# Kernel optimization log

Measured on AMD Instinct MI355X. Metric: run time of the kernel, lower is better.

Reference implementation:

```python
import jax, jax.numpy as jnp
import numpy as np

N = 50000      # nodes
E = 800000     # edges (avg degree 16)
G = 128        # graphs in batch
IN = 128       # in_channels
H = 128        # hidden_dim
C = 10         # num_classes


def setup_inputs() -> dict:
    key = jax.random.key(0)
    ks = jax.random.split(key, 8)
    x = jax.random.normal(ks[0], (N, IN), dtype=jnp.float32)
    edge_index = jax.random.randint(ks[1], (2, E), 0, N)
    edge_attr = jax.random.uniform(ks[2], (E,), dtype=jnp.float32)
    batch = jnp.sort(jax.random.randint(ks[3], (N,), 0, G))
    def glorot(k, fan_in, fan_out):
        return jax.random.normal(k, (fan_in, fan_out), dtype=jnp.float32) / np.float32(np.sqrt(fan_in))
    return {
        "x": x,
        "edge_index": edge_index,
        "edge_attr": edge_attr,
        "batch": batch,
        "W1": glorot(ks[4], IN, H), "b1": jnp.zeros((H,), jnp.float32),
        "W2": glorot(ks[5], H, H), "b2": jnp.zeros((H,), jnp.float32),
        "W3": glorot(ks[6], H, C), "b3": jnp.zeros((C,), jnp.float32),
    }


def gcn_conv(x, src, dst, ew, W, b, n):
    # symmetric GCN normalization (self-loops already appended, weight 1)
    deg = jax.ops.segment_sum(ew, dst, num_segments=n)            # [N]
    dinv = jnp.where(deg > 0, jax.lax.rsqrt(deg), 0.0)
    norm = dinv[src] * ew * dinv[dst]                             # [E+N]
    h = x @ W                                                     # [N, out]
    agg = jax.ops.segment_sum(h[src] * norm[:, None], dst, num_segments=n)
    return agg + b


def reference(x, edge_index, edge_attr, batch, W1, b1, W2, b2, W3, b3):
    n = x.shape[0]
    loop = jnp.arange(n)
    src = jnp.concatenate([edge_index[0], loop])
    dst = jnp.concatenate([edge_index[1], loop])
    ew = jnp.concatenate([edge_attr, jnp.ones((n,), edge_attr.dtype)])
    h = jax.nn.relu(gcn_conv(x, src, dst, ew, W1, b1, n))   # dropout is identity in eval
    h = jax.nn.relu(gcn_conv(h, src, dst, ew, W2, b2, n))
    h = gcn_conv(h, src, dst, ew, W3, b3, n)                 # [N, C]
    # global mean pool over graphs
    sums = jax.ops.segment_sum(h, batch, num_segments=G)     # [G, C]
    cnt = jax.ops.segment_sum(jnp.ones((n,), h.dtype), batch, num_segments=G)
    pooled = sums / jnp.maximum(cnt, 1.0)[:, None]
    return jax.nn.log_softmax(pooled, axis=1)
```

## Files before the change

kernel.cpp:

```cpp
#include <hip/hip_runtime.h>

#define NN 50000
#define NE 800000
#define NG 128
#define DIM 128
#define CO 10
#define CAP 64
#define NB 2048

typedef unsigned long long ull;
typedef unsigned short ushort;
typedef unsigned int uint;

static __device__ __forceinline__ ushort f2bf(float f) {
    uint u = __float_as_uint(f);
    uint r = (u + 0x7FFF + ((u >> 16) & 1)) >> 16;
    return (ushort)r;
}
#define EWS (1.0f / 65535.0f)

__global__ void k_ell(const int* __restrict__ src, const int* __restrict__ dst,
                      const float* __restrict__ ew, int* __restrict__ cnt,
                      uint* __restrict__ ell) {
    int e = blockIdx.x * blockDim.x + threadIdx.x;
    if (e >= NE) return;
    int d = dst[e], s = src[e];
    int slot = atomicAdd(&cnt[d], 1);
    if (slot < CAP) {
        uint w16 = (uint)__float2uint_rn(ew[e] * 65535.0f);
        ell[(size_t)d * CAP + slot] = (w16 << 16) | (uint)s;
    }
}

__global__ __launch_bounds__(256) void k_deg(const int* __restrict__ cnt,
                                             const uint* __restrict__ ell,
                                             float* __restrict__ dinv) {
    int node = blockIdx.x * 4 + (threadIdx.x >> 6);
    int lane = threadIdx.x & 63;
    if (node >= NN) return;
    int n = cnt[node];
    float w = 0.0f;
    if (lane < n) w = (float)(ell[(size_t)node * CAP + lane] >> 16) * EWS;
#pragma unroll
    for (int off = 32; off; off >>= 1) w += __shfl_down(w, off);
    if (lane == 0) dinv[node] = rsqrtf(1.0f + w);
}

__global__ __launch_bounds__(256) void k_gemm128(const void* __restrict__ Ain, int abf,
                                                 const float* __restrict__ W,
                                                 const float* __restrict__ dinv,
                                                 ushort* __restrict__ C, int M) {
    __shared__ float As[64][33];
    __shared__ float Bs[32][132];
    int tid = threadIdx.x;
    int block_row = blockIdx.x * 64;
    int tx = tid & 15;
    int ty = tid >> 4;
    int r0 = ty * 4;
    int c1 = tx * 4, c2 = 64 + tx * 4;
    float acc[4][8];
#pragma unroll
    for (int i = 0; i < 4; i++)
#pragma unroll
        for (int j = 0; j < 8; j++) acc[i][j] = 0.0f;

    for (int k0 = 0; k0 < 128; k0 += 32) {
        if (abf) {
            const ushort* Ab = (const ushort*)Ain;
            int ar = tid >> 2;
            int ac = (tid & 3) * 8;
            int grow = block_row + ar;
            if (grow >= M) grow = M - 1;
            uint4 v = *(const uint4*)&Ab[(size_t)grow * 128 + k0 + ac];
            As[ar][ac + 0] = __uint_as_float(v.x << 16);
            As[ar][ac + 1] = __uint_as_float(v.x & 0xffff0000u);
            As[ar][ac + 2] = __uint_as_float(v.y << 16);
            As[ar][ac + 3] = __uint_as_float(v.y & 0xffff0000u);
            As[ar][ac + 4] = __uint_as_float(v.z << 16);
            As[ar][ac + 5] = __uint_as_float(v.z & 0xffff0000u);
            As[ar][ac + 6] = __uint_as_float(v.w << 16);
            As[ar][ac + 7] = __uint_as_float(v.w & 0xffff0000u);
        } else {
            const float* Af = (const float*)Ain;
#pragma unroll
            for (int l = 0; l < 2; l++) {
                int idx = tid + l * 256;
                int ar = idx >> 3;
                int ac = (idx & 7) * 4;
                int grow = block_row + ar;
                if (grow >= M) grow = M - 1;
                float4 v = *(const float4*)&Af[(size_t)grow * 128 + k0 + ac];
                As[ar][ac + 0] = v.x; As[ar][ac + 1] = v.y;
                As[ar][ac + 2] = v.z; As[ar][ac + 3] = v.w;
            }
        }
#pragma unroll
        for (int l = 0; l < 4; l++) {
            int idx = tid + l * 256;
            int br = idx >> 5;
            int bc = (idx & 31) * 4;
            float4 v = *(const float4*)&W[(size_t)(k0 + br) * 128 + bc];
            *(float4*)&Bs[br][bc] = v;
        }
        __syncthreads();
#pragma unroll
        for (int kk = 0; kk < 32; kk++) {
            float a0 = As[r0 + 0][kk];
            float a1 = As[r0 + 1][kk];
            float a2 = As[r0 + 2][kk];
            float a3 = As[r0 + 3][kk];
            float4 bl = *(float4*)&Bs[kk][c1];
            float4 bh = *(float4*)&Bs[kk][c2];
            acc[0][0] += a0 * bl.x; acc[0][1] += a0 * bl.y; acc[0][2] += a0 * bl.z; acc[0][3] += a0 * bl.w;
            acc[0][4] += a0 * bh.x; acc[0][5] += a0 * bh.y; acc[0][6] += a0 * bh.z; acc[0][7] += a0 * bh.w;
            acc[1][0] += a1 * bl.x; acc[1][1] += a1 * bl.y; acc[1][2] += a1 * bl.z; acc[1][3] += a1 * bl.w;
            acc[1][4] += a1 * bh.x; acc[1][5] += a1 * bh.y; acc[1][6] += a1 * bh.z; acc[1][7] += a1 * bh.w;
            acc[2][0] += a2 * bl.x; acc[2][1] += a2 * bl.y; acc[2][2] += a2 * bl.z; acc[2][3] += a2 * bl.w;
            acc[2][4] += a2 * bh.x; acc[2][5] += a2 * bh.y; acc[2][6] += a2 * bh.z; acc[2][7] += a2 * bh.w;
            acc[3][0] += a3 * bl.x; acc[3][1] += a3 * bl.y; acc[3][2] += a3 * bl.z; acc[3][3] += a3 * bl.w;
            acc[3][4] += a3 * bh.x; acc[3][5] += a3 * bh.y; acc[3][6] += a3 * bh.z; acc[3][7] += a3 * bh.w;
        }
        __syncthreads();
    }
#pragma unroll
    for (int i = 0; i < 4; i++) {
        int grow = block_row + r0 + i;
        if (grow < M) {
            float di = dinv[grow];
            ushort4 u1, u2;
            u1.x = f2bf(di * acc[i][0]); u1.y = f2bf(di * acc[i][1]);
            u1.z = f2bf(di * acc[i][2]); u1.w = f2bf(di * acc[i][3]);
            u2.x = f2bf(di * acc[i][4]); u2.y = f2bf(di * acc[i][5]);
            u2.z = f2bf(di * acc[i][6]); u2.w = f2bf(di * acc[i][7]);
            *(ushort4*)&C[(size_t)grow * 128 + c1] = u1;
            *(ushort4*)&C[(size_t)grow * 128 + c2] = u2;
        }
    }
}

__global__ __launch_bounds__(256) void k_gemm10(const ushort* __restrict__ A,
                                                const float* __restrict__ W3,
                                                const float* __restrict__ dinv,
                                                float* __restrict__ C3, int M) {
    __shared__ float Ws[1280];
    int tid = threadIdx.x;
    for (int i = tid; i < 1280; i += 256) Ws[i] = W3[i];
    __syncthreads();
    int col = tid & 15;
    int rloc = tid >> 4;
    int row = blockIdx.x * 16 + rloc;
    if (row >= M || col >= 10) return;
    const ushort* a = &A[(size_t)row * 128];
    float acc = 0.0f;
#pragma unroll
    for (int k = 0; k < 128; k += 4) {
        ushort4 av = *(const ushort4*)&a[k];
        acc += __uint_as_float((uint)av.x << 16) * Ws[(k + 0) * 10 + col];
        acc += __uint_as_float((uint)av.y << 16) * Ws[(k + 1) * 10 + col];
        acc += __uint_as_float((uint)av.z << 16) * Ws[(k + 2) * 10 + col];
        acc += __uint_as_float((uint)av.w << 16) * Ws[(k + 3) * 10 + col];
    }
    C3[(size_t)row * 10 + col] = dinv[row] * acc;
}

__global__ __launch_bounds__(256) void k_gather128(const int* __restrict__ cnt,
                                                   const uint* __restrict__ ell,
                                                   const float* __restrict__ dinv,
                                                   const ushort* __restrict__ h,
                                                   const float* __restrict__ b,
                                                   ushort* __restrict__ outp) {
    int node = blockIdx.x * 4 + (threadIdx.x >> 6);
    int lane = threadIdx.x & 63;
    if (node >= NN) return;
    int n = cnt[node];
    uint hp = *(const uint*)&h[(size_t)node * 128 + lane * 2];
    float ax = __uint_as_float(hp << 16);
    float ay = __uint_as_float(hp & 0xffff0000u);
    uint rec = ell[(size_t)node * CAP + lane];
    int ce = (int)(rec & 0xffffu);
    float we = (float)(rec >> 16) * EWS;
    int j = 0;
    for (; j + 3 < n; j += 4) {
        int s0 = __shfl(ce, j + 0), s1 = __shfl(ce, j + 1);
        int s2 = __shfl(ce, j + 2), s3 = __shfl(ce, j + 3);
        float w0 = __shfl(we, j + 0), w1 = __shfl(we, j + 1);
        float w2 = __shfl(we, j + 2), w3 = __shfl(we, j + 3);
        uint p0 = *(const uint*)&h[(size_t)s0 * 128 + lane * 2];
        uint p1 = *(const uint*)&h[(size_t)s1 * 128 + lane * 2];
        uint p2 = *(const uint*)&h[(size_t)s2 * 128 + lane * 2];
        uint p3 = *(const uint*)&h[(size_t)s3 * 128 + lane * 2];
        ax += w0 * __uint_as_float(p0 << 16) + w1 * __uint_as_float(p1 << 16)
            + w2 * __uint_as_float(p2 << 16) + w3 * __uint_as_float(p3 << 16);
        ay += w0 * __uint_as_float(p0 & 0xffff0000u) + w1 * __uint_as_float(p1 & 0xffff0000u)
            + w2 * __uint_as_float(p2 & 0xffff0000u) + w3 * __uint_as_float(p3 & 0xffff0000u);
    }
    for (; j < n; j++) {
        int s0 = __shfl(ce, j);
        float w0 = __shfl(we, j);
        uint p0 = *(const uint*)&h[(size_t)s0 * 128 + lane * 2];
        ax += w0 * __uint_as_float(p0 << 16);
        ay += w0 * __uint_as_float(p0 & 0xffff0000u);
    }
    float di = dinv[node];
    ax = fmaxf(di * ax + b[lane * 2 + 0], 0.0f);
    ay = fmaxf(di * ay + b[lane * 2 + 1], 0.0f);
    uint o = ((uint)f2bf(ay) << 16) | (uint)f2bf(ax);
    *(uint*)&outp[(size_t)node * 128 + lane * 2] = o;
}

__global__ __launch_bounds__(256) void k_pool_node(const int* __restrict__ cnt,
                                                   const uint* __restrict__ ell,
                                                   const float* __restrict__ dinv,
                                                   const float* __restrict__ z,
                                                   const int* __restrict__ batch,
                                                   float* __restrict__ partial) {
    __shared__ float ls[NG * CO + NG];
    for (int i = threadIdx.x; i < NG * CO + NG; i += 256) ls[i] = 0.0f;
    __syncthreads();
    int lane = threadIdx.x & 63;
    int gwave = blockIdx.x * 4 + (threadIdx.x >> 6);
    for (int node = gwave; node < NN; node += NB * 4) {
        int n = cnt[node];
        float w = 0.0f; int s = 0;
        if (lane < n) {
            uint rec = ell[(size_t)node * CAP + lane];
            s = (int)(rec & 0xffffu);
            w = (float)(rec >> 16) * EWS;
        } else if (lane == n) {
            s = node;
            w = 1.0f;
        }
        const float* zp = &z[(size_t)s * 10];
        float v[10];
#pragma unroll
        for (int f = 0; f < 10; f++) v[f] = w * zp[f];
#pragma unroll
        for (int off = 32; off; off >>= 1) {
#pragma unroll
            for (int f = 0; f < 10; f++) v[f] += __shfl_down(v[f], off);
        }
        if (lane == 0) {
            int g = batch[node];
            float di = dinv[node];
            float* lp = &ls[g * 10];
#pragma unroll
            for (int f = 0; f < 10; f++) atomicAdd(&lp[f], di * v[f]);
            atomicAdd(&ls[NG * CO + g], 1.0f);
        }
    }
    __syncthreads();
    float* pb = &partial[(size_t)blockIdx.x * (NG * CO + NG)];
    for (int i = threadIdx.x; i < NG * CO + NG; i += 256) pb[i] = ls[i];
}

__global__ __launch_bounds__(256) void k_pool_final(const float* __restrict__ partial,
                                                    const float* __restrict__ b3,
                                                    float* __restrict__ out) {
    __shared__ float red[4][11];
    int g = blockIdx.x;
    int t = threadIdx.x;
    int lane = t & 63, wv = t >> 6;
    float v[10]; float c = 0.0f;
#pragma unroll
    for (int f = 0; f < 10; f++) v[f] = 0.0f;
    for (int b = t; b < NB; b += 256) {
        const float* pb = &partial[(size_t)b * (NG * CO + NG)];
#pragma unroll
        for (int f = 0; f < 10; f++) v[f] += pb[g * 10 + f];
        c += pb[NG * CO + g];
    }
#pragma unroll
    for (int off = 32; off; off >>= 1) {
#pragma unroll
        for (int f = 0; f < 10; f++) v[f] += __shfl_down(v[f], off);
        c += __shfl_down(c, off);
    }
    if (lane == 0) {
#pragma unroll
        for (int f = 0; f < 10; f++) red[wv][f] = v[f];
        red[wv][10] = c;
    }
    __syncthreads();
    if (t == 0) {
        float p[10], m = -1e30f;
        float cc = red[0][10] + red[1][10] + red[2][10] + red[3][10];
        cc = fmaxf(cc, 1.0f);
#pragma unroll
        for (int f = 0; f < 10; f++) {
            p[f] = (red[0][f] + red[1][f] + red[2][f] + red[3][f]) / cc + b3[f];
            m = fmaxf(m, p[f]);
        }
        float ssum = 0.0f;
#pragma unroll
        for (int f = 0; f < 10; f++) ssum += __expf(p[f] - m);
        float lse = m + __logf(ssum);
#pragma unroll
        for (int f = 0; f < 10; f++) out[g * 10 + f] = p[f] - lse;
    }
}

extern "C" void kernel_launch(void* const* d_in, const int* in_sizes, int n_in,
                              void* d_out, int out_size, void* d_ws, size_t ws_size,
                              hipStream_t stream) {
    const float* x     = (const float*)d_in[0];
    const int*   ei    = (const int*)d_in[1];
    const float* ea    = (const float*)d_in[2];
    const int*   batch = (const int*)d_in[3];
    const float* W1    = (const float*)d_in[4];
    const float* b1    = (const float*)d_in[5];
    const float* W2    = (const float*)d_in[6];
    const float* b2    = (const float*)d_in[7];
    const float* W3    = (const float*)d_in[8];
    const float* b3    = (const float*)d_in[9];
    float* out = (float*)d_out;
    float* ws  = (float*)d_ws;

    const int* esrc = ei;
    const int* edst = ei + NE;

    ushort* hb      = (ushort*)ws;
    ushort* gb      = (ushort*)(ws + 3200000);
    float*  z       = ws + 6400000;
    float*  dinv    = ws + 6900000;
    int*    cnt     = (int*)(ws + 6950000);
    uint*   ell     = (uint*)(ws + 7000000);
    float*  partial = (float*)hb;

    hipMemsetAsync(cnt, 0, NN * sizeof(int), stream);
    k_ell<<<(NE + 255) / 256, 256, 0, stream>>>(esrc, edst, ea, cnt, ell);
    k_deg<<<(NN + 3) / 4, 256, 0, stream>>>(cnt, ell, dinv);

    k_gemm128<<<(NN + 63) / 64, 256, 0, stream>>>(x, 0, W1, dinv, hb, NN);
    k_gather128<<<(NN + 3) / 4, 256, 0, stream>>>(cnt, ell, dinv, hb, b1, gb);

    k_gemm128<<<(NN + 63) / 64, 256, 0, stream>>>(gb, 1, W2, dinv, hb, NN);
    k_gather128<<<(NN + 3) / 4, 256, 0, stream>>>(cnt, ell, dinv, hb, b2, gb);

    k_gemm10<<<(NN + 15) / 16, 256, 0, stream>>>(gb, W3, dinv, z, NN);
    k_pool_node<<<NB, 256, 0, stream>>>(cnt, ell, dinv, z, batch, partial);
    k_pool_final<<<NG, 256, 0, stream>>>(partial, b3, out);
}
```

Measured before the change: 325.7 us.

## Replace FP32 SIMT GEMM with bf16 MFMA GEMM using pre-transposed weights

Swaps the shared-memory tiled FP32 GEMM for a matrix-core kernel that uses the 16x16x32 bf16 MFMA instruction, with operands loaded straight from global memory. Two small kernels convert W1 and W2 into transposed bf16 copies in workspace so each lane can load contiguous 8-element B fragments. The first layer's fp32 input is rounded to bf16 in registers, which lowers precision. Output stores become scalar 16-bit writes per lane instead of vectorized ones.

```diff
diff --git a/kernel.cpp b/kernel.cpp
--- a/kernel.cpp
+++ b/kernel.cpp
@@ -11,6 +11,8 @@
 typedef unsigned long long ull;
 typedef unsigned short ushort;
 typedef unsigned int uint;
+typedef __attribute__((ext_vector_type(8))) short short8;
+typedef __attribute__((ext_vector_type(4))) float floatx4;
 
 static __device__ __forceinline__ ushort f2bf(float f) {
     uint u = __float_as_uint(f);
@@ -46,94 +48,58 @@
     if (lane == 0) dinv[node] = rsqrtf(1.0f + w);
 }
 
-__global__ __launch_bounds__(256) void k_gemm128(const void* __restrict__ Ain, int abf,
-                                                 const float* __restrict__ W,
-                                                 const float* __restrict__ dinv,
-                                                 ushort* __restrict__ C, int M) {
-    __shared__ float As[64][33];
-    __shared__ float Bs[32][132];
-    int tid = threadIdx.x;
-    int block_row = blockIdx.x * 64;
-    int tx = tid & 15;
-    int ty = tid >> 4;
-    int r0 = ty * 4;
-    int c1 = tx * 4, c2 = 64 + tx * 4;
-    float acc[4][8];
-#pragma unroll
-    for (int i = 0; i < 4; i++)
-#pragma unroll
-        for (int j = 0; j < 8; j++) acc[i][j] = 0.0f;
-
-    for (int k0 = 0; k0 < 128; k0 += 32) {
+__global__ void k_prepw(const float* __restrict__ W, ushort* __restrict__ Wt) {
+    int i = blockIdx.x * blockDim.x + threadIdx.x;
+    int k = i >> 7, n = i & 127;
+    Wt[n * 128 + k] = f2bf(W[i]);
+}
+
+__global__ __launch_bounds__(256) void k_gemm_mfma(const void* __restrict__ Ain, int abf,
+                                                   const ushort* __restrict__ Wt,
+                                                   const float* __restrict__ dinv,
+                                                   ushort* __restrict__ C, int M) {
+    int wave = threadIdx.x >> 6;
+    int lane = threadIdx.x & 63;
+    int quad = lane >> 4;
+    int mcol = lane & 15;
+    int r0 = blockIdx.x * 64 + wave * 16;
+    int arow = r0 + mcol;
+    if (arow >= M) arow = M - 1;
+    floatx4 acc[8];
+#pragma unroll
+    for (int t = 0; t < 8; t++) acc[t] = (floatx4){0.0f, 0.0f, 0.0f, 0.0f};
+
+    const ushort* Ab = (const ushort*)Ain;
+    const float*  Af = (const float*)Ain;
+#pragma unroll
+    for (int kk = 0; kk < 4; kk++) {
+        int koff = kk * 32 + quad * 8;
+        short8 a;
         if (abf) {
-            const ushort* Ab = (const ushort*)Ain;
-            int ar = tid >> 2;
-            int ac = (tid & 3) * 8;
-            int grow = block_row + ar;
-            if (grow >= M) grow = M - 1;
-            uint4 v = *(const uint4*)&Ab[(size_t)grow * 128 + k0 + ac];
-            As[ar][ac + 0] = __uint_as_float(v.x << 16);
-            As[ar][ac + 1] = __uint_as_float(v.x & 0xffff0000u);
-            As[ar][ac + 2] = __uint_as_float(v.y << 16);
-            As[ar][ac + 3] = __uint_as_float(v.y & 0xffff0000u);
-            As[ar][ac + 4] = __uint_as_float(v.z << 16);
-            As[ar][ac + 5] = __uint_as_float(v.z & 0xffff0000u);
-            As[ar][ac + 6] = __uint_as_float(v.w << 16);
-            As[ar][ac + 7] = __uint_as_float(v.w & 0xffff0000u);
+            a = *(const short8*)&Ab[(size_t)arow * 128 + koff];
         } else {
-            const float* Af = (const float*)Ain;
-#pragma unroll
-            for (int l = 0; l < 2; l++) {
-                int idx = tid + l * 256;
-                int ar = idx >> 3;
-                int ac = (idx & 7) * 4;
-                int grow = block_row + ar;
-                if (grow >= M) grow = M - 1;
-                float4 v = *(const float4*)&Af[(size_t)grow * 128 + k0 + ac];
-                As[ar][ac + 0] = v.x; As[ar][ac + 1] = v.y;
-                As[ar][ac + 2] = v.z; As[ar][ac + 3] = v.w;
-            }
-        }
-#pragma unroll
-        for (int l = 0; l < 4; l++) {
-            int idx = tid + l * 256;
-            int br = idx >> 5;
-            int bc = (idx & 31) * 4;
-            float4 v = *(const float4*)&W[(size_t)(k0 + br) * 128 + bc];
-            *(float4*)&Bs[br][bc] = v;
-        }
-        __syncthreads();
-#pragma unroll
-        for (int kk = 0; kk < 32; kk++) {
-            float a0 = As[r0 + 0][kk];
-            float a1 = As[r0 + 1][kk];
-            float a2 = As[r0 + 2][kk];
-            float a3 = As[r0 + 3][kk];
-            float4 bl = *(float4*)&Bs[kk][c1];
-            float4 bh = *(float4*)&Bs[kk][c2];
-            acc[0][0] += a0 * bl.x; acc[0][1] += a0 * bl.y; acc[0][2] += a0 * bl.z; acc[0][3] += a0 * bl.w;
-            acc[0][4] += a0 * bh.x; acc[0][5] += a0 * bh.y; acc[0][6] += a0 * bh.z; acc[0][7] += a0 * bh.w;
-            acc[1][0] += a1 * bl.x; acc[1][1] += a1 * bl.y; acc[1][2] += a1 * bl.z; acc[1][3] += a1 * bl.w;
-            acc[1][4] += a1 * bh.x; acc[1][5] += a1 * bh.y; acc[1][6] += a1 * bh.z; acc[1][7] += a1 * bh.w;
-            acc[2][0] += a2 * bl.x; acc[2][1] += a2 * bl.y; acc[2][2] += a2 * bl.z; acc[2][3] += a2 * bl.w;
-            acc[2][4] += a2 * bh.x; acc[2][5] += a2 * bh.y; acc[2][6] += a2 * bh.z; acc[2][7] += a2 * bh.w;
-            acc[3][0] += a3 * bl.x; acc[3][1] += a3 * bl.y; acc[3][2] += a3 * bl.z; acc[3][3] += a3 * bl.w;
-            acc[3][4] += a3 * bh.x; acc[3][5] += a3 * bh.y; acc[3][6] += a3 * bh.z; acc[3][7] += a3 * bh.w;
-        }
-        __syncthreads();
-    }
-#pragma unroll
-    for (int i = 0; i < 4; i++) {
-        int grow = block_row + r0 + i;
-        if (grow < M) {
-            float di = dinv[grow];
-            ushort4 u1, u2;
-            u1.x = f2bf(di * acc[i][0]); u1.y = f2bf(di * acc[i][1]);
-            u1.z = f2bf(di * acc[i][2]); u1.w = f2bf(di * acc[i][3]);
-            u2.x = f2bf(di * acc[i][4]); u2.y = f2bf(di * acc[i][5]);
-            u2.z = f2bf(di * acc[i][6]); u2.w = f2bf(di * acc[i][7]);
-            *(ushort4*)&C[(size_t)grow * 128 + c1] = u1;
-            *(ushort4*)&C[(size_t)grow * 128 + c2] = u2;
+            const float* ap = &Af[(size_t)arow * 128 + koff];
+            float4 x0 = *(const float4*)ap;
+            float4 x1 = *(const float4*)(ap + 4);
+            union { short8 v; ushort u[8]; } ua;
+            ua.u[0] = f2bf(x0.x); ua.u[1] = f2bf(x0.y); ua.u[2] = f2bf(x0.z); ua.u[3] = f2bf(x0.w);
+            ua.u[4] = f2bf(x1.x); ua.u[5] = f2bf(x1.y); ua.u[6] = f2bf(x1.z); ua.u[7] = f2bf(x1.w);
+            a = ua.v;
+        }
+#pragma unroll
+        for (int t = 0; t < 8; t++) {
+            short8 b = *(const short8*)&Wt[(size_t)(t * 16 + mcol) * 128 + koff];
+            acc[t] = __builtin_amdgcn_mfma_f32_16x16x32_bf16(a, b, acc[t], 0, 0, 0);
+        }
+    }
+#pragma unroll
+    for (int reg = 0; reg < 4; reg++) {
+        int row = r0 + quad * 4 + reg;
+        if (row < M) {
+            float di = dinv[row];
+            ushort* cp = &C[(size_t)row * 128];
+#pragma unroll
+            for (int t = 0; t < 8; t++) cp[t * 16 + mcol] = f2bf(di * acc[t][reg]);
         }
     }
 }
@@ -324,16 +290,20 @@
     float*  dinv    = ws + 6900000;
     int*    cnt     = (int*)(ws + 6950000);
     uint*   ell     = (uint*)(ws + 7000000);
+    ushort* wt1     = (ushort*)(ws + 10200000);
+    ushort* wt2     = (ushort*)(ws + 10210000);
     float*  partial = (float*)hb;
 
     hipMemsetAsync(cnt, 0, NN * sizeof(int), stream);
     k_ell<<<(NE + 255) / 256, 256, 0, stream>>>(esrc, edst, ea, cnt, ell);
+    k_prepw<<<64, 256, 0, stream>>>(W1, wt1);
+    k_prepw<<<64, 256, 0, stream>>>(W2, wt2);
     k_deg<<<(NN + 3) / 4, 256, 0, stream>>>(cnt, ell, dinv);
 
-    k_gemm128<<<(NN + 63) / 64, 256, 0, stream>>>(x, 0, W1, dinv, hb, NN);
+    k_gemm_mfma<<<(NN + 63) / 64, 256, 0, stream>>>(x, 0, wt1, dinv, hb, NN);
     k_gather128<<<(NN + 3) / 4, 256, 0, stream>>>(cnt, ell, dinv, hb, b1, gb);
 
-    k_gemm128<<<(NN + 63) / 64, 256, 0, stream>>>(gb, 1, W2, dinv, hb, NN);
+    k_gemm_mfma<<<(NN + 63) / 64, 256, 0, stream>>>(gb, 1, wt2, dinv, hb, NN);
     k_gather128<<<(NN + 3) / 4, 256, 0, stream>>>(cnt, ell, dinv, hb, b2, gb);
 
     k_gemm10<<<(NN + 15) / 16, 256, 0, stream>>>(gb, W3, dinv, z, NN);
```

New measurement: 312.5 us. 1.04x faster.
